# Kernel optimization log

Hardware: AMD Instinct MI355X
Metric: run time of the kernel (lower is better)

The kernel has to match this reference:

```python
import jax, jax.numpy as jnp
import numpy as np

BZ, T, D, DFF, E, BEAMS = 128, 32, 768, 3072, 8, 2


def setup_inputs() -> dict:
    key = jax.random.key(0)
    ks = jax.random.split(key, 4)
    s = 0.02
    return {
        "x": jax.random.normal(ks[0], (BZ, T, D), jnp.float32),
        "attention_mask": jnp.ones((BZ, T), jnp.float32),
        "Wg": jax.random.normal(ks[1], (D, E), jnp.float32) * s,   # gate Linear(D,E,bias=False)
        "W1": jax.random.normal(ks[2], (E, D, DFF), jnp.float32) * s,
        "b1": jnp.zeros((E, DFF), jnp.float32),
        "W2": jax.random.normal(ks[3], (E, DFF, D), jnp.float32) * s,
        "b2": jnp.zeros((E, D), jnp.float32),
    }


def reference(x, attention_mask, Wg, W1, b1, W2, b2):
    # forward_gate: module builds its own all-ones mask regardless of input mask
    mask = jnp.ones((x.shape[0], x.shape[1]), x.dtype)
    x_avg = (x * mask[..., None]).sum(1) / mask[..., None].sum(1)   # [bz, D]
    prob = jax.nn.softmax(x_avg @ Wg, axis=-1)                       # [bz, E]
    # beam_search (layer_judge='first', pre-route): topk on exp(log(softmax)) == softmax probs
    scores = jnp.exp(jnp.log(prob))
    topv, topi = jax.lax.top_k(scores, BEAMS)                        # [bz, beams]
    beam_scores = topv.reshape(-1)                                   # [bz*beams]
    expert_route = topi.reshape(-1, 1)                                # [bz*beams, 1]
    sel = expert_route[:, -1]
    # replicate x per beam: [bz*beams, T, D]
    x_rep = jnp.broadcast_to(x[:, None], (x.shape[0], BEAMS, x.shape[1], x.shape[2]))
    x_rep = x_rep.reshape(-1, x.shape[1], x.shape[2])
    # per-sample expert FFN dispatch (dense masked loop over the E=8 experts)
    out = jnp.zeros_like(x_rep)
    for e in range(E):
        h = jax.nn.gelu(jnp.einsum('nsd,df->nsf', x_rep, W1[e]) + b1[e], approximate=False)
        ye = jnp.einsum('nsf,fd->nsd', h, W2[e]) + b2[e]
        out = jnp.where((sel == e)[:, None, None], ye, out)
    return (out, beam_scores, expert_route)
```

## Files before the change

### kernel.cpp

```cpp
#include <hip/hip_runtime.h>
#include <cstddef>
#include <cstdint>

#define BZd   128
#define Td    32
#define Dd    768
#define DFFd  3072
#define Ed    8
#define NBEAM 256
#define ROWS_TOT 8192
#define OUT_ELEMS 6291456
#define MAXTILES 72
#define MAXT2    40

typedef unsigned short u16;
typedef __attribute__((ext_vector_type(4))) unsigned short ushort4v;
typedef __attribute__((ext_vector_type(8))) short frag_ab;
typedef __attribute__((ext_vector_type(4))) float floatx4;

__device__ __forceinline__ u16 f2bf(float f) {
  unsigned int u = __builtin_bit_cast(unsigned int, f);
  u += 0x7FFFu + ((u >> 16) & 1u);
  return (u16)(u >> 16);
}

__device__ __forceinline__ void async_copy16(u16* lds, const u16* g) {
  __builtin_amdgcn_global_load_lds(
      (const __attribute__((address_space(1))) void*)g,
      (__attribute__((address_space(3))) void*)lds, 16, 0, 0);
}

__device__ __forceinline__ float gelu_fast(float x) {
  float z = 1.5957691216f * (x + 0.044715f * x * x * x);
  return x / (1.0f + __expf(-z));
}

__global__ __launch_bounds__(256) void route_kernel(
    const float* __restrict__ x, const float* __restrict__ Wg,
    float* __restrict__ out, int* __restrict__ sel) {
  int b = blockIdx.x;
  int t = threadIdx.x;
  __shared__ float red[256][8];
  float la[8];
#pragma unroll
  for (int e = 0; e < 8; e++) la[e] = 0.f;
  for (int d = t; d < Dd; d += 256) {
    const float* xp = x + (size_t)b * Td * Dd + d;
    float xa = 0.f;
#pragma unroll
    for (int tt = 0; tt < Td; tt++) xa += xp[(size_t)tt * Dd];
    xa *= (1.0f / 32.0f);
#pragma unroll
    for (int e = 0; e < 8; e++) la[e] += xa * Wg[d * 8 + e];
  }
#pragma unroll
  for (int e = 0; e < 8; e++) red[t][e] = la[e];
  __syncthreads();
  for (int s = 128; s > 0; s >>= 1) {
    if (t < s) {
#pragma unroll
      for (int e = 0; e < 8; e++) red[t][e] += red[t + s][e];
    }
    __syncthreads();
  }
  if (t == 0) {
    float lg[8];
#pragma unroll
    for (int e = 0; e < 8; e++) lg[e] = red[0][e];
    float mx = lg[0];
#pragma unroll
    for (int e = 1; e < 8; e++) mx = fmaxf(mx, lg[e]);
    float p[8];
    float sum = 0.f;
#pragma unroll
    for (int e = 0; e < 8; e++) { p[e] = __expf(lg[e] - mx); sum += p[e]; }
    float inv = 1.0f / sum;
#pragma unroll
    for (int e = 0; e < 8; e++) p[e] *= inv;
    int i0 = 0; float v0 = p[0];
#pragma unroll
    for (int e = 1; e < 8; e++) if (p[e] > v0) { v0 = p[e]; i0 = e; }
    int i1 = -1; float v1 = -1.0f;
#pragma unroll
    for (int e = 0; e < 8; e++) if (e != i0 && p[e] > v1) { v1 = p[e]; i1 = e; }
    float* bs = out + OUT_ELEMS;
    float* er = out + OUT_ELEMS + NBEAM;
    bs[2 * b] = v0; bs[2 * b + 1] = v1;
    er[2 * b] = (float)i0; er[2 * b + 1] = (float)i1;
    sel[2 * b] = i0; sel[2 * b + 1] = i1;
  }
}

__global__ __launch_bounds__(256) void bucket_kernel(
    const int* __restrict__ sel, int* __restrict__ perm,
    int4* __restrict__ tiles, int4* __restrict__ tiles2) {
  __shared__ int ssel[NBEAM];
  __shared__ int scnt[8];
  __shared__ int soff[8];
  __shared__ int scur[8];
  __shared__ int sperm[NBEAM];
  int t = threadIdx.x;
  ssel[t] = sel[t];
  __syncthreads();
  if (t == 0) {
    for (int e = 0; e < 8; e++) scnt[e] = 0;
    for (int n = 0; n < NBEAM; n++) scnt[ssel[n]]++;
    int o = 0;
    for (int e = 0; e < 8; e++) { soff[e] = o; scur[e] = o; o += scnt[e]; }
    for (int n = 0; n < NBEAM; n++) { int e = ssel[n]; sperm[scur[e]++] = n; }
    int tt = 0;
    for (int e = 0; e < 8; e++) {
      int nr = scnt[e] * 32;
      int base = soff[e] * 32;
      for (int r0 = 0; r0 < nr; r0 += 128) {
        tiles[tt] = make_int4(e, base + r0, min(128, nr - r0), 0);
        tt++;
      }
    }
    for (; tt < MAXTILES; tt++) tiles[tt] = make_int4(-1, 0, 0, 0);
    int t2 = 0;
    for (int e = 0; e < 8; e++) {
      int nr = scnt[e] * 32;
      int base = soff[e] * 32;
      for (int r0 = 0; r0 < nr; r0 += 256) {
        tiles2[t2] = make_int4(e, base + r0, min(256, nr - r0), 0);
        t2++;
      }
    }
    for (; t2 < MAXT2; t2++) tiles2[t2] = make_int4(-1, 0, 0, 0);
  }
  __syncthreads();
  perm[t] = sperm[t];
}

__global__ __launch_bounds__(256) void convert_x_kernel(
    const float* __restrict__ x, u16* __restrict__ xbf) {
  size_t i = ((size_t)blockIdx.x * 256 + threadIdx.x) * 4;
  float4 v = *(const float4*)(x + i);
  ushort4v pv = {f2bf(v.x), f2bf(v.y), f2bf(v.z), f2bf(v.w)};
  *(ushort4v*)(xbf + i) = pv;
}

__global__ __launch_bounds__(256) void transpose_bf16_kernel(
    const float* __restrict__ in, u16* __restrict__ out, int row0, int col0,
    int ld_in, size_t estr_in, int ld_out, size_t estr_out) {
  __shared__ u16 tile[64][65];
  int e = blockIdx.z;
  int r0 = blockIdx.x * 64, c0 = blockIdx.y * 64;
  int t = threadIdx.x;
  int rr = t >> 4, cc4 = (t & 15) * 4;
  const float* ip = in + (size_t)e * estr_in + (size_t)(row0 + r0) * ld_in + col0 + c0;
#pragma unroll
  for (int i = 0; i < 4; i++) {
    int r = rr + 16 * i;
    float4 v = *(const float4*)(ip + (size_t)r * ld_in + cc4);
    tile[r][cc4 + 0] = f2bf(v.x);
    tile[r][cc4 + 1] = f2bf(v.y);
    tile[r][cc4 + 2] = f2bf(v.z);
    tile[r][cc4 + 3] = f2bf(v.w);
  }
  __syncthreads();
  int ccw = t >> 4, r4 = (t & 15) * 4;
  u16* op = out + (size_t)e * estr_out + (size_t)c0 * ld_out + r0;
#pragma unroll
  for (int i = 0; i < 4; i++) {
    int cc = ccw + 16 * i;
    ushort4v pv = {tile[r4 + 0][cc], tile[r4 + 1][cc], tile[r4 + 2][cc], tile[r4 + 3][cc]};
    *(ushort4v*)(op + (size_t)cc * ld_out + r4) = pv;
  }
}

__global__ __launch_bounds__(512, 2) void gemm1_kernel(
    const u16* __restrict__ xbf, const u16* __restrict__ w1t,
    const float* __restrict__ b1, const int* __restrict__ perm,
    const int4* __restrict__ tiles2, u16* __restrict__ h, int f0, int FC) {
  int4 meta = tiles2[blockIdx.y];
  int e = meta.x;
  if (e < 0) return;
  int grow0 = meta.y, nrows = meta.z;
  int bx = blockIdx.x;

  extern __shared__ __align__(16) u16 smem[];
  u16* As = smem;
  u16* Bs = smem + 32768;

  int t = threadIdx.x;
  int l = t & 63;
  int wid = t >> 6;
  int wr = wid >> 2;
  int wc = wid & 3;
  int lrow = l & 15, lquad = l >> 4;

  const u16* ag[4]; const u16* bg[4];
  int ldst[4];
#pragma unroll
  for (int j = 0; j < 4; j++) {
    int s = j * 512 + t;
    int m = s >> 3;
    int koff = ((s & 7) ^ ((m >> 1) & 7)) * 8;
    int gr = grow0 + m;
    int bidx = gr >> 5; bidx = bidx < NBEAM ? bidx : NBEAM - 1;
    int batch = perm[bidx] >> 1;
    ag[j] = xbf + ((size_t)batch * Td + (m & 31)) * Dd + koff;
    bg[j] = w1t + ((size_t)e * FC + bx * 256 + m) * Dd + koff;
    ldst[j] = j * 4096 + t * 8;
  }

  int swz = (lrow >> 1) & 7;
  int ca0 = (lquad ^ swz) * 8, ca1 = ((lquad + 4) ^ swz) * 8;
  int abase0 = (wr * 128 + lrow) * 64 + ca0;
  int abase1 = (wr * 128 + lrow) * 64 + ca1;
  int bbase0 = (wc * 64 + lrow) * 64 + ca0;
  int bbase1 = (wc * 64 + lrow) * 64 + ca1;

  floatx4 acc[8][4];
#pragma unroll
  for (int mi = 0; mi < 8; mi++)
#pragma unroll
    for (int ni = 0; ni < 4; ni++) acc[mi][ni] = (floatx4){0.f, 0.f, 0.f, 0.f};

  const int nk = Dd / 64;

#pragma unroll
  for (int j = 0; j < 4; j++) { async_copy16(As + ldst[j], ag[j]); ag[j] += 64; }
#pragma unroll
  for (int j = 0; j < 4; j++) { async_copy16(Bs + ldst[j], bg[j]); bg[j] += 64; }

  for (int kt = 0; kt < nk; kt++) {
    const int b = kt & 1;
    const u16* Ab = As + b * 16384;
    const u16* Bb = Bs + b * 16384;
    const int pd = (b ^ 1) * 16384;
    const bool pre = (kt + 1 < nk);

    frag_ab af[4], bfr[4];

    if (pre) {
      async_copy16(As + pd + ldst[0], ag[0]); ag[0] += 64;
      async_copy16(As + pd + ldst[1], ag[1]); ag[1] += 64;
      asm volatile("s_waitcnt vmcnt(2)\n\ts_barrier" ::: "memory");
    } else {
      asm volatile("s_waitcnt vmcnt(0)\n\ts_barrier" ::: "memory");
    }
#pragma unroll
    for (int i = 0; i < 4; i++) bfr[i] = *(const frag_ab*)(Bb + bbase0 + i * 1024);
#pragma unroll
    for (int i = 0; i < 4; i++) af[i] = *(const frag_ab*)(Ab + abase0 + i * 1024);
    __builtin_amdgcn_s_setprio(1);
#pragma unroll
    for (int mi = 0; mi < 4; mi++)
#pragma unroll
      for (int ni = 0; ni < 4; ni++)
        acc[mi][ni] = __builtin_amdgcn_mfma_f32_16x16x32_bf16(bfr[ni], af[mi], acc[mi][ni], 0, 0, 0);
    __builtin_amdgcn_s_setprio(0);

    if (pre) {
      async_copy16(As + pd + ldst[2], ag[2]); ag[2] += 64;
      async_copy16(As + pd + ldst[3], ag[3]); ag[3] += 64;
    }
#pragma unroll
    for (int i = 0; i < 4; i++) af[i] = *(const frag_ab*)(Ab + abase0 + (i + 4) * 1024);
    __builtin_amdgcn_s_setprio(1);
#pragma unroll
    for (int mi = 0; mi < 4; mi++)
#pragma unroll
      for (int ni = 0; ni < 4; ni++)
        acc[mi + 4][ni] = __builtin_amdgcn_mfma_f32_16x16x32_bf16(bfr[ni], af[mi], acc[mi + 4][ni], 0, 0, 0);
    __builtin_amdgcn_s_setprio(0);

    if (pre) {
      async_copy16(Bs + pd + ldst[0], bg[0]); bg[0] += 64;
      async_copy16(Bs + pd + ldst[1], bg[1]); bg[1] += 64;
    }
#pragma unroll
    for (int i = 0; i < 4; i++) bfr[i] = *(const frag_ab*)(Bb + bbase1 + i * 1024);
#pragma unroll
    for (int i = 0; i < 4; i++) af[i] = *(const frag_ab*)(Ab + abase1 + i * 1024);
    __builtin_amdgcn_s_setprio(1);
#pragma unroll
    for (int mi = 0; mi < 4; mi++)
#pragma unroll
      for (int ni = 0; ni < 4; ni++)
        acc[mi][ni] = __builtin_amdgcn_mfma_f32_16x16x32_bf16(bfr[ni], af[mi], acc[mi][ni], 0, 0, 0);
    __builtin_amdgcn_s_setprio(0);

    if (pre) {
      async_copy16(Bs + pd + ldst[2], bg[2]); bg[2] += 64;
      async_copy16(Bs + pd + ldst[3], bg[3]); bg[3] += 64;
    }
#pragma unroll
    for (int i = 0; i < 4; i++) af[i] = *(const frag_ab*)(Ab + abase1 + (i + 4) * 1024);
    __builtin_amdgcn_s_setprio(1);
#pragma unroll
    for (int mi = 0; mi < 4; mi++)
#pragma unroll
      for (int ni = 0; ni < 4; ni++)
        acc[mi + 4][ni] = __builtin_amdgcn_mfma_f32_16x16x32_bf16(bfr[ni], af[mi], acc[mi + 4][ni], 0, 0, 0);
    __builtin_amdgcn_s_setprio(0);

    asm volatile("s_barrier" ::: "memory");
  }

#pragma unroll
  for (int mi = 0; mi < 8; mi++) {
    int row = wr * 128 + mi * 16 + lrow;
    if (row < nrows) {
      u16* hp = h + (size_t)(grow0 + row) * FC + bx * 256 + wc * 64 + lquad * 4;
      const float* bp = b1 + (size_t)e * DFFd + f0 + bx * 256 + wc * 64 + lquad * 4;
#pragma unroll
      for (int ni = 0; ni < 4; ni++) {
        float4 bias = *(const float4*)(bp + ni * 16);
        ushort4v pv = {f2bf(gelu_fast(acc[mi][ni][0] + bias.x)),
                       f2bf(gelu_fast(acc[mi][ni][1] + bias.y)),
                       f2bf(gelu_fast(acc[mi][ni][2] + bias.z)),
                       f2bf(gelu_fast(acc[mi][ni][3] + bias.w))};
        *(ushort4v*)(hp + ni * 16) = pv;
      }
    }
  }
}

__global__ __launch_bounds__(256) void gemm2_kernel(
    const u16* __restrict__ h, const u16* __restrict__ w2t,
    const float* __restrict__ b2, const int* __restrict__ perm,
    const int4* __restrict__ tiles, float* __restrict__ out,
    int FC, int first) {
  int4 meta = tiles[blockIdx.y];
  int e = meta.x;
  if (e < 0) return;
  int grow0 = meta.y, nrows = meta.z;
  int bx = blockIdx.x;

  __shared__ __align__(16) u16 As[2 * 128 * 64];
  __shared__ __align__(16) u16 Bs[2 * 128 * 64];
  __shared__ int sbeam[4];

  int t = threadIdx.x;
  if (t < 4) {
    int idx = (grow0 >> 5) + t;
    sbeam[t] = perm[idx < NBEAM ? idx : NBEAM - 1];
  }
  __syncthreads();

  int l = t & 63, w = t >> 6;
  int wm = w & 1, wn = w >> 1;
  int lrow = l & 15, lquad = l >> 4;

  const u16* ag[4]; const u16* bg[4];
  u16* al[4]; u16* bl[4];
#pragma unroll
  for (int j = 0; j < 4; j++) {
    int s = j * 256 + t;
    int m = s >> 3;
    int koff = (((s & 7) ^ ((m >> 1) & 7))) * 8;
    int arow = grow0 + m;
    arow = arow < ROWS_TOT ? arow : ROWS_TOT - 1;
    ag[j] = h + (size_t)arow * FC + koff;
    bg[j] = w2t + ((size_t)e * Dd + bx * 128 + m) * FC + koff;
    al[j] = As + j * 2048 + w * 512;
    bl[j] = Bs + j * 2048 + w * 512;
  }

  int aoff[2][4], boff[2][4];
#pragma unroll
  for (int hh = 0; hh < 2; hh++)
#pragma unroll
    for (int i = 0; i < 4; i++) {
      int ra = wm * 64 + i * 16 + lrow;
      aoff[hh][i] = ra * 64 + (((lquad + hh * 4) ^ ((ra >> 1) & 7)) * 8);
      int rb = wn * 64 + i * 16 + lrow;
      boff[hh][i] = rb * 64 + (((lquad + hh * 4) ^ ((rb >> 1) & 7)) * 8);
    }

  floatx4 acc[4][4];
#pragma unroll
  for (int mi = 0; mi < 4; mi++)
#pragma unroll
    for (int ni = 0; ni < 4; ni++) acc[mi][ni] = (floatx4){0.f, 0.f, 0.f, 0.f};

  const int nk = FC / 64;
#pragma unroll
  for (int j = 0; j < 4; j++) {
    async_copy16(al[j], ag[j]);
    async_copy16(bl[j], bg[j]);
    ag[j] += 64; bg[j] += 64;
  }

#pragma unroll 2
  for (int kt = 0; kt < nk; kt++) {
    const int cur = kt & 1;
    if (kt + 1 < nk) {
#pragma unroll
      for (int j = 0; j < 4; j++) {
        async_copy16(al[j] + (cur ^ 1) * 8192, ag[j]);
        async_copy16(bl[j] + (cur ^ 1) * 8192, bg[j]);
        ag[j] += 64; bg[j] += 64;
      }
      asm volatile("s_waitcnt vmcnt(8)\n\ts_barrier" ::: "memory");
    } else {
      asm volatile("s_waitcnt vmcnt(0)\n\ts_barrier" ::: "memory");
    }
    const u16* Ab = As + cur * 8192;
    const u16* Bb = Bs + cur * 8192;
#pragma unroll
    for (int hh = 0; hh < 2; hh++) {
      frag_ab af[4], bfr[4];
#pragma unroll
      for (int mi = 0; mi < 4; mi++) af[mi] = *(const frag_ab*)(Ab + aoff[hh][mi]);
#pragma unroll
      for (int ni = 0; ni < 4; ni++) bfr[ni] = *(const frag_ab*)(Bb + boff[hh][ni]);
      __builtin_amdgcn_s_setprio(1);
#pragma unroll
      for (int mi = 0; mi < 4; mi++)
#pragma unroll
        for (int ni = 0; ni < 4; ni++)
          acc[mi][ni] = __builtin_amdgcn_mfma_f32_16x16x32_bf16(bfr[ni], af[mi], acc[mi][ni], 0, 0, 0);
      __builtin_amdgcn_s_setprio(0);
    }
    asm volatile("s_barrier" ::: "memory");
  }

#pragma unroll
  for (int mi = 0; mi < 4; mi++) {
    int row = wm * 64 + mi * 16 + lrow;
    if (row < nrows) {
      int beam = sbeam[row >> 5];
      float* op = out + ((size_t)beam * Td + (row & 31)) * Dd + bx * 128 + wn * 64 + lquad * 4;
      const float* bp = b2 + (size_t)e * Dd + bx * 128 + wn * 64 + lquad * 4;
#pragma unroll
      for (int ni = 0; ni < 4; ni++) {
        if (first) {
          float4 bias = *(const float4*)(bp + ni * 16);
          float4 v = {acc[mi][ni][0] + bias.x, acc[mi][ni][1] + bias.y,
                      acc[mi][ni][2] + bias.z, acc[mi][ni][3] + bias.w};
          *(float4*)(op + ni * 16) = v;
        } else {
          float4 o = *(float4*)(op + ni * 16);
          o.x += acc[mi][ni][0]; o.y += acc[mi][ni][1];
          o.z += acc[mi][ni][2]; o.w += acc[mi][ni][3];
          *(float4*)(op + ni * 16) = o;
        }
      }
    }
  }
}

extern "C" void kernel_launch(void* const* d_in, const int* in_sizes, int n_in,
                              void* d_out, int out_size, void* d_ws, size_t ws_size,
                              hipStream_t stream) {
  const float* x  = (const float*)d_in[0];
  const float* Wg = (const float*)d_in[2];
  const float* W1 = (const float*)d_in[3];
  const float* b1 = (const float*)d_in[4];
  const float* W2 = (const float*)d_in[5];
  const float* b2 = (const float*)d_in[6];
  float* out = (float*)d_out;

  char* ws = (char*)d_ws;
  int*  sel    = (int*)ws;
  int*  perm   = sel + NBEAM;
  int4* tiles  = (int4*)(ws + 4096);
  int4* tiles2 = (int4*)(ws + 6144);

  const size_t xbf_off = 65536;
  const size_t xbf_bytes = (size_t)BZd * Td * Dd * 2;
  int FC = 768;
  if      (xbf_off + xbf_bytes + (size_t)40960 * 3072 <= ws_size) FC = 3072;
  else if (xbf_off + xbf_bytes + (size_t)40960 * 1536 <= ws_size) FC = 1536;
  int NC = DFFd / FC;

  u16* xbf = (u16*)(ws + xbf_off);
  u16* w1t = (u16*)(ws + xbf_off + xbf_bytes);
  u16* w2t = w1t + (size_t)Ed * FC * Dd;
  u16* h   = w2t + (size_t)Ed * Dd * FC;

  static bool attr_done = false;
  if (!attr_done) {
    hipFuncSetAttribute(reinterpret_cast<const void*>(gemm1_kernel),
                        hipFuncAttributeMaxDynamicSharedMemorySize, 131072);
    attr_done = true;
  }

  route_kernel<<<BZd, 256, 0, stream>>>(x, Wg, out, sel);
  bucket_kernel<<<1, 256, 0, stream>>>(sel, perm, tiles, tiles2);
  convert_x_kernel<<<(BZd * Td * Dd) / 1024, 256, 0, stream>>>(x, xbf);

  for (int c = 0; c < NC; c++) {
    transpose_bf16_kernel<<<dim3(Dd / 64, FC / 64, Ed), 256, 0, stream>>>(
        W1, w1t, 0, c * FC, DFFd, (size_t)Dd * DFFd, Dd, (size_t)FC * Dd);
    transpose_bf16_kernel<<<dim3(FC / 64, Dd / 64, Ed), 256, 0, stream>>>(
        W2, w2t, c * FC, 0, Dd, (size_t)DFFd * Dd, FC, (size_t)Dd * FC);
    gemm1_kernel<<<dim3(FC / 256, MAXT2), 512, 131072, stream>>>(
        xbf, w1t, b1, perm, tiles2, h, c * FC, FC);
    gemm2_kernel<<<dim3(Dd / 128, MAXTILES), 256, 0, stream>>>(
        h, w2t, b2, perm, tiles, out, FC, c == 0 ? 1 : 0);
  }
}
```

Baseline: 366.4 us.

## Enlarge gemm2 tiles to 256x256 with 512 threads and interleaved prefetch

Rewrites the second expert GEMM to use 256-row by 256-column tiles (reusing the gemm1 tile list), 8 waves per block and 128 KB of dynamic shared memory, matching the gemm1 structure. The next k-slice's async copies are split into four chunks interleaved between MFMA phases instead of issued all at once. The goal is more operand reuse per byte loaded and better latency hiding. In exchange the grid has fewer blocks, there is more padding waste for partially filled expert tiles, and the larger register and LDS footprint lowers occupancy.

```diff
diff --git a/kernel.cpp b/kernel.cpp
--- a/kernel.cpp
+++ b/kernel.cpp
@@ -320,113 +320,151 @@
   }
 }
 
-__global__ __launch_bounds__(256) void gemm2_kernel(
+__global__ __launch_bounds__(512, 2) void gemm2_kernel(
     const u16* __restrict__ h, const u16* __restrict__ w2t,
     const float* __restrict__ b2, const int* __restrict__ perm,
-    const int4* __restrict__ tiles, float* __restrict__ out,
+    const int4* __restrict__ tiles2, float* __restrict__ out,
     int FC, int first) {
-  int4 meta = tiles[blockIdx.y];
+  int4 meta = tiles2[blockIdx.y];
   int e = meta.x;
   if (e < 0) return;
   int grow0 = meta.y, nrows = meta.z;
   int bx = blockIdx.x;
 
-  __shared__ __align__(16) u16 As[2 * 128 * 64];
-  __shared__ __align__(16) u16 Bs[2 * 128 * 64];
-  __shared__ int sbeam[4];
+  extern __shared__ __align__(16) u16 smem[];
+  u16* As = smem;
+  u16* Bs = smem + 32768;
+  __shared__ int sbeam[8];
 
   int t = threadIdx.x;
-  if (t < 4) {
+  if (t < 8) {
     int idx = (grow0 >> 5) + t;
     sbeam[t] = perm[idx < NBEAM ? idx : NBEAM - 1];
   }
   __syncthreads();
 
-  int l = t & 63, w = t >> 6;
-  int wm = w & 1, wn = w >> 1;
+  int l = t & 63;
+  int wid = t >> 6;
+  int wr = wid >> 2;
+  int wc = wid & 3;
   int lrow = l & 15, lquad = l >> 4;
 
   const u16* ag[4]; const u16* bg[4];
-  u16* al[4]; u16* bl[4];
+  int ldst[4];
 #pragma unroll
   for (int j = 0; j < 4; j++) {
-    int s = j * 256 + t;
+    int s = j * 512 + t;
     int m = s >> 3;
-    int koff = (((s & 7) ^ ((m >> 1) & 7))) * 8;
+    int koff = ((s & 7) ^ ((m >> 1) & 7)) * 8;
     int arow = grow0 + m;
     arow = arow < ROWS_TOT ? arow : ROWS_TOT - 1;
     ag[j] = h + (size_t)arow * FC + koff;
-    bg[j] = w2t + ((size_t)e * Dd + bx * 128 + m) * FC + koff;
-    al[j] = As + j * 2048 + w * 512;
-    bl[j] = Bs + j * 2048 + w * 512;
-  }
-
-  int aoff[2][4], boff[2][4];
-#pragma unroll
-  for (int hh = 0; hh < 2; hh++)
-#pragma unroll
-    for (int i = 0; i < 4; i++) {
-      int ra = wm * 64 + i * 16 + lrow;
-      aoff[hh][i] = ra * 64 + (((lquad + hh * 4) ^ ((ra >> 1) & 7)) * 8);
-      int rb = wn * 64 + i * 16 + lrow;
-      boff[hh][i] = rb * 64 + (((lquad + hh * 4) ^ ((rb >> 1) & 7)) * 8);
-    }
-
-  floatx4 acc[4][4];
-#pragma unroll
-  for (int mi = 0; mi < 4; mi++)
+    bg[j] = w2t + ((size_t)e * Dd + bx * 256 + m) * FC + koff;
+    ldst[j] = j * 4096 + t * 8;
+  }
+
+  int swz = (lrow >> 1) & 7;
+  int ca0 = (lquad ^ swz) * 8, ca1 = ((lquad + 4) ^ swz) * 8;
+  int abase0 = (wr * 128 + lrow) * 64 + ca0;
+  int abase1 = (wr * 128 + lrow) * 64 + ca1;
+  int bbase0 = (wc * 64 + lrow) * 64 + ca0;
+  int bbase1 = (wc * 64 + lrow) * 64 + ca1;
+
+  floatx4 acc[8][4];
+#pragma unroll
+  for (int mi = 0; mi < 8; mi++)
 #pragma unroll
     for (int ni = 0; ni < 4; ni++) acc[mi][ni] = (floatx4){0.f, 0.f, 0.f, 0.f};
 
   const int nk = FC / 64;
-#pragma unroll
-  for (int j = 0; j < 4; j++) {
-    async_copy16(al[j], ag[j]);
-    async_copy16(bl[j], bg[j]);
-    ag[j] += 64; bg[j] += 64;
-  }
-
-#pragma unroll 2
+
+#pragma unroll
+  for (int j = 0; j < 4; j++) { async_copy16(As + ldst[j], ag[j]); ag[j] += 64; }
+#pragma unroll
+  for (int j = 0; j < 4; j++) { async_copy16(Bs + ldst[j], bg[j]); bg[j] += 64; }
+
   for (int kt = 0; kt < nk; kt++) {
-    const int cur = kt & 1;
-    if (kt + 1 < nk) {
-#pragma unroll
-      for (int j = 0; j < 4; j++) {
-        async_copy16(al[j] + (cur ^ 1) * 8192, ag[j]);
-        async_copy16(bl[j] + (cur ^ 1) * 8192, bg[j]);
-        ag[j] += 64; bg[j] += 64;
-      }
-      asm volatile("s_waitcnt vmcnt(8)\n\ts_barrier" ::: "memory");
+    const int b = kt & 1;
+    const u16* Ab = As + b * 16384;
+    const u16* Bb = Bs + b * 16384;
+    const int pd = (b ^ 1) * 16384;
+    const bool pre = (kt + 1 < nk);
+
+    frag_ab af[4], bfr[4];
+
+    if (pre) {
+      async_copy16(As + pd + ldst[0], ag[0]); ag[0] += 64;
+      async_copy16(As + pd + ldst[1], ag[1]); ag[1] += 64;
+      asm volatile("s_waitcnt vmcnt(2)\n\ts_barrier" ::: "memory");
     } else {
       asm volatile("s_waitcnt vmcnt(0)\n\ts_barrier" ::: "memory");
     }
-    const u16* Ab = As + cur * 8192;
-    const u16* Bb = Bs + cur * 8192;
-#pragma unroll
-    for (int hh = 0; hh < 2; hh++) {
-      frag_ab af[4], bfr[4];
-#pragma unroll
-      for (int mi = 0; mi < 4; mi++) af[mi] = *(const frag_ab*)(Ab + aoff[hh][mi]);
-#pragma unroll
-      for (int ni = 0; ni < 4; ni++) bfr[ni] = *(const frag_ab*)(Bb + boff[hh][ni]);
-      __builtin_amdgcn_s_setprio(1);
-#pragma unroll
-      for (int mi = 0; mi < 4; mi++)
-#pragma unroll
-        for (int ni = 0; ni < 4; ni++)
-          acc[mi][ni] = __builtin_amdgcn_mfma_f32_16x16x32_bf16(bfr[ni], af[mi], acc[mi][ni], 0, 0, 0);
-      __builtin_amdgcn_s_setprio(0);
-    }
+#pragma unroll
+    for (int i = 0; i < 4; i++) bfr[i] = *(const frag_ab*)(Bb + bbase0 + i * 1024);
+#pragma unroll
+    for (int i = 0; i < 4; i++) af[i] = *(const frag_ab*)(Ab + abase0 + i * 1024);
+    __builtin_amdgcn_s_setprio(1);
+#pragma unroll
+    for (int mi = 0; mi < 4; mi++)
+#pragma unroll
+      for (int ni = 0; ni < 4; ni++)
+        acc[mi][ni] = __builtin_amdgcn_mfma_f32_16x16x32_bf16(bfr[ni], af[mi], acc[mi][ni], 0, 0, 0);
+    __builtin_amdgcn_s_setprio(0);
+
+    if (pre) {
+      async_copy16(As + pd + ldst[2], ag[2]); ag[2] += 64;
+      async_copy16(As + pd + ldst[3], ag[3]); ag[3] += 64;
+    }
+#pragma unroll
+    for (int i = 0; i < 4; i++) af[i] = *(const frag_ab*)(Ab + abase0 + (i + 4) * 1024);
+    __builtin_amdgcn_s_setprio(1);
+#pragma unroll
+    for (int mi = 0; mi < 4; mi++)
+#pragma unroll
+      for (int ni = 0; ni < 4; ni++)
+        acc[mi + 4][ni] = __builtin_amdgcn_mfma_f32_16x16x32_bf16(bfr[ni], af[mi], acc[mi + 4][ni], 0, 0, 0);
+    __builtin_amdgcn_s_setprio(0);
+
+    if (pre) {
+      async_copy16(Bs + pd + ldst[0], bg[0]); bg[0] += 64;
+      async_copy16(Bs + pd + ldst[1], bg[1]); bg[1] += 64;
+    }
+#pragma unroll
+    for (int i = 0; i < 4; i++) bfr[i] = *(const frag_ab*)(Bb + bbase1 + i * 1024);
+#pragma unroll
+    for (int i = 0; i < 4; i++) af[i] = *(const frag_ab*)(Ab + abase1 + i * 1024);
+    __builtin_amdgcn_s_setprio(1);
+#pragma unroll
+    for (int mi = 0; mi < 4; mi++)
+#pragma unroll
+      for (int ni = 0; ni < 4; ni++)
+        acc[mi][ni] = __builtin_amdgcn_mfma_f32_16x16x32_bf16(bfr[ni], af[mi], acc[mi][ni], 0, 0, 0);
+    __builtin_amdgcn_s_setprio(0);
+
+    if (pre) {
+      async_copy16(Bs + pd + ldst[2], bg[2]); bg[2] += 64;
+      async_copy16(Bs + pd + ldst[3], bg[3]); bg[3] += 64;
+    }
+#pragma unroll
+    for (int i = 0; i < 4; i++) af[i] = *(const frag_ab*)(Ab + abase1 + (i + 4) * 1024);
+    __builtin_amdgcn_s_setprio(1);
+#pragma unroll
+    for (int mi = 0; mi < 4; mi++)
+#pragma unroll
+      for (int ni = 0; ni < 4; ni++)
+        acc[mi + 4][ni] = __builtin_amdgcn_mfma_f32_16x16x32_bf16(bfr[ni], af[mi], acc[mi + 4][ni], 0, 0, 0);
+    __builtin_amdgcn_s_setprio(0);
+
     asm volatile("s_barrier" ::: "memory");
   }
 
 #pragma unroll
-  for (int mi = 0; mi < 4; mi++) {
-    int row = wm * 64 + mi * 16 + lrow;
+  for (int mi = 0; mi < 8; mi++) {
+    int row = wr * 128 + mi * 16 + lrow;
     if (row < nrows) {
       int beam = sbeam[row >> 5];
-      float* op = out + ((size_t)beam * Td + (row & 31)) * Dd + bx * 128 + wn * 64 + lquad * 4;
-      const float* bp = b2 + (size_t)e * Dd + bx * 128 + wn * 64 + lquad * 4;
+      float* op = out + ((size_t)beam * Td + (row & 31)) * Dd + bx * 256 + wc * 64 + lquad * 4;
+      const float* bp = b2 + (size_t)e * Dd + bx * 256 + wc * 64 + lquad * 4;
 #pragma unroll
       for (int ni = 0; ni < 4; ni++) {
         if (first) {
@@ -478,6 +516,8 @@
   if (!attr_done) {
     hipFuncSetAttribute(reinterpret_cast<const void*>(gemm1_kernel),
                         hipFuncAttributeMaxDynamicSharedMemorySize, 131072);
+    hipFuncSetAttribute(reinterpret_cast<const void*>(gemm2_kernel),
+                        hipFuncAttributeMaxDynamicSharedMemorySize, 131072);
     attr_done = true;
   }
 
@@ -492,7 +532,7 @@
         W2, w2t, c * FC, 0, Dd, (size_t)DFFd * Dd, FC, (size_t)Dd * FC);
     gemm1_kernel<<<dim3(FC / 256, MAXT2), 512, 131072, stream>>>(
         xbf, w1t, b1, perm, tiles2, h, c * FC, FC);
-    gemm2_kernel<<<dim3(Dd / 128, MAXTILES), 256, 0, stream>>>(
-        h, w2t, b2, perm, tiles, out, FC, c == 0 ? 1 : 0);
-  }
-}
+    gemm2_kernel<<<dim3(Dd / 256, MAXT2), 512, 131072, stream>>>(
+        h, w2t, b2, perm, tiles2, out, FC, c == 0 ? 1 : 0);
+  }
+}
```

Result: slower. 377.0 us (+2.9%).
